# Optimization experiments

Measured on AMD Instinct MI355X. Metric: run time of the kernel, lower is better.

## Reference

```python
import jax, jax.numpy as jnp
import numpy as np

TTOT, CHANS = 65536, 64
WLEN, ETAS, WTIME = 25, 25, 0.36


def setup_inputs() -> dict:
    key = jax.random.key(0)
    k1, k2, k3 = jax.random.split(key, 3)
    inputs = jax.random.normal(k1, (TTOT, CHANS), dtype=jnp.float32)
    # layer weights: RandomNormal(mean=0, stddev=50), shape (etas, 1)
    a = jax.random.normal(k2, (ETAS, 1), dtype=jnp.float32) * 50.0
    b = jax.random.normal(k3, (ETAS, 1), dtype=jnp.float32) * 50.0
    return {"inputs": inputs, "a": a, "b": b}


def reference(inputs, a, b):
    # inputs: (ttot, chans); a, b: (etas, 1)
    etas = a.shape[0]
    chans = inputs.shape[1]
    t = jnp.linspace(-1.0, 1.0, WLEN).astype(inputs.dtype) * WTIME  # (wlen,)
    # Morlet wavelet bank: exp(-a^2 t^2 / 2) * cos(2*pi*b*t) -> (etas, wlen)
    win = jnp.exp(-(a ** 2) * (t ** 2) * 0.5) * jnp.cos(2.0 * jnp.pi * b * t)
    win = win[:, ::-1]  # np.convolve flips the kernel (window is symmetric; kept for fidelity)
    # Depthwise 'valid' conv: each channel convolved with all etas filters.
    lhs = inputs.T[None]  # (1, chans, ttot)
    rhs = jnp.broadcast_to(win[None], (chans, etas, WLEN)).reshape(chans * etas, 1, WLEN)
    out = jax.lax.conv_general_dilated(
        lhs, rhs, window_strides=(1,), padding='VALID',
        dimension_numbers=('NCH', 'OIH', 'NCH'),
        feature_group_count=chans,
    )  # (1, chans*etas, L)
    L = out.shape[-1]
    return out.reshape(chans, etas, L).transpose(2, 1, 0)  # (L, etas, chans)
```

## Files before the change

kernel.cpp:

```cpp
#include <hip/hip_runtime.h>
#include <cstddef>

constexpr int TTOT  = 65536;
constexpr int CHANS = 64;
constexpr int WLEN  = 25;
constexpr int ETAS  = 25;
constexpr int LOUT  = TTOT - WLEN + 1;
constexpr int LT    = 52;
constexpr int ROWS  = LT + WLEN - 1;
constexpr int NBLK  = (LOUT + LT - 1) / LT;

__global__ void win_kernel(const float* __restrict__ a,
                           const float* __restrict__ b,
                           float* __restrict__ win) {
    int idx = blockIdx.x * blockDim.x + threadIdx.x;
    if (idx >= ETAS * WLEN) return;
    int e = idx / WLEN;
    int k = idx - e * WLEN;
    float t  = (float)(k - 12) * 0.03f;
    float ae = a[e];
    float be = b[e];
    float g  = expf(-0.5f * ae * ae * t * t);
    float c  = cosf(6.28318530717958647692f * be * t);
    win[idx] = g * c;
}

__global__ __launch_bounds__(256) void conv_kernel(
    const float* __restrict__ in,
    const float* __restrict__ win,
    float* __restrict__ out) {
    __shared__ float xs[ROWS * CHANS];

    const int l0 = blockIdx.x * LT;

    {
        const float4* in4 = reinterpret_cast<const float4*>(in + (size_t)l0 * CHANS);
        float4* xs4 = reinterpret_cast<float4*>(xs);
        constexpr int N4 = (ROWS * CHANS) / 4;
        for (int i4 = threadIdx.x; i4 < N4; i4 += 256) {
            int r = i4 >> 4;
            float4 v = make_float4(0.f, 0.f, 0.f, 0.f);
            if (l0 + r < TTOT) v = in4[i4];
            xs4[i4] = v;
        }
    }
    __syncthreads();

    const int c  = threadIdx.x & 63;
    const int ls = threadIdx.x >> 6;

    for (int li = ls; li < LT; li += 4) {
        const int l = l0 + li;
        if (l >= LOUT) break;

        float x[WLEN];
#pragma unroll
        for (int k = 0; k < WLEN; ++k)
            x[k] = xs[(li + k) * CHANS + c];

        const size_t obase = (size_t)l * (ETAS * CHANS) + c;
        for (int e = 0; e < ETAS; ++e) {
            const float* w = win + e * WLEN;
            float acc = 0.f;
#pragma unroll
            for (int k = 0; k < WLEN; ++k)
                acc = fmaf(x[k], w[k], acc);
            out[obase + (size_t)(e * CHANS)] = acc;
        }
    }
}

extern "C" void kernel_launch(void* const* d_in, const int* in_sizes, int n_in,
                              void* d_out, int out_size, void* d_ws, size_t ws_size,
                              hipStream_t stream) {
    const float* in = (const float*)d_in[0];
    const float* a  = (const float*)d_in[1];
    const float* b  = (const float*)d_in[2];
    float* out = (float*)d_out;
    float* win = (float*)d_ws;

    win_kernel<<<(ETAS * WLEN + 255) / 256, 256, 0, stream>>>(a, b, win);
    conv_kernel<<<NBLK, 256, 0, stream>>>(in, win, out);
}
```

Measured before the change: 463.4 us.

## Register-block conv with sliding input window per wave, drop shared memory

Each wave now owns a tile of 13 consecutive output positions and loads a 37-tap input window per channel straight into registers from global memory, removing the shared-memory staging and block barrier. The loop order is inverted so each filter's 25 weights are loaded once and reused across 13 outputs, cutting per-output weight loads. This raises register pressure (37 inputs plus 25 weights), which may lower occupancy. The kernel is likely bound by the large output write in any case.

New measurement: 448.9 us. 3.1% less time.

```diff
diff --git a/kernel.cpp b/kernel.cpp
--- a/kernel.cpp
+++ b/kernel.cpp
@@ -6,9 +6,11 @@
 constexpr int WLEN  = 25;
 constexpr int ETAS  = 25;
 constexpr int LOUT  = TTOT - WLEN + 1;
-constexpr int LT    = 52;
-constexpr int ROWS  = LT + WLEN - 1;
-constexpr int NBLK  = (LOUT + LT - 1) / LT;
+constexpr int LPW   = 13;
+constexpr int TAPS  = LPW + WLEN - 1;
+constexpr int WPB   = 4;
+constexpr int NTILE = (LOUT + LPW - 1) / LPW;
+constexpr int NBLK  = (NTILE + WPB - 1) / WPB;
 
 __global__ void win_kernel(const float* __restrict__ a,
                            const float* __restrict__ b,
@@ -29,43 +31,37 @@
     const float* __restrict__ in,
     const float* __restrict__ win,
     float* __restrict__ out) {
-    __shared__ float xs[ROWS * CHANS];
+    const int c    = threadIdx.x & 63;
+    const int wv   = threadIdx.x >> 6;
+    const int tile = blockIdx.x * WPB + wv;
+    const int lBase = tile * LPW;
+    if (lBase >= LOUT) return;
 
-    const int l0 = blockIdx.x * LT;
+    float x[TAPS];
+#pragma unroll
+    for (int r = 0; r < TAPS; ++r) {
+        int row = lBase + r;
+        if (row > TTOT - 1) row = TTOT - 1;
+        x[r] = in[(size_t)row * CHANS + c];
+    }
 
-    {
-        const float4* in4 = reinterpret_cast<const float4*>(in + (size_t)l0 * CHANS);
-        float4* xs4 = reinterpret_cast<float4*>(xs);
-        constexpr int N4 = (ROWS * CHANS) / 4;
-        for (int i4 = threadIdx.x; i4 < N4; i4 += 256) {
-            int r = i4 >> 4;
-            float4 v = make_float4(0.f, 0.f, 0.f, 0.f);
-            if (l0 + r < TTOT) v = in4[i4];
-            xs4[i4] = v;
-        }
-    }
-    __syncthreads();
+    const int lrem = LOUT - lBase;
 
-    const int c  = threadIdx.x & 63;
-    const int ls = threadIdx.x >> 6;
+#pragma unroll 1
+    for (int e = 0; e < ETAS; ++e) {
+        float w[WLEN];
+#pragma unroll
+        for (int k = 0; k < WLEN; ++k) w[k] = win[e * WLEN + k];
 
-    for (int li = ls; li < LT; li += 4) {
-        const int l = l0 + li;
-        if (l >= LOUT) break;
-
-        float x[WLEN];
+        float* op = out + (size_t)lBase * (ETAS * CHANS) + e * CHANS + c;
 #pragma unroll
-        for (int k = 0; k < WLEN; ++k)
-            x[k] = xs[(li + k) * CHANS + c];
-
-        const size_t obase = (size_t)l * (ETAS * CHANS) + c;
-        for (int e = 0; e < ETAS; ++e) {
-            const float* w = win + e * WLEN;
+        for (int j = 0; j < LPW; ++j) {
             float acc = 0.f;
 #pragma unroll
             for (int k = 0; k < WLEN; ++k)
-                acc = fmaf(x[k], w[k], acc);
-            out[obase + (size_t)(e * CHANS)] = acc;
+                acc = fmaf(x[j + k], w[k], acc);
+            if (j < lrem)
+                op[(size_t)j * (ETAS * CHANS)] = acc;
         }
     }
 }
```
